# Performance work log

Hardware: AMD Instinct MI355X
Metric: run time of the kernel (lower is better)

## Reference

```python
import jax, jax.numpy as jnp
import numpy as np

D = 1024
H = 16
DH = D // H
F = 4096
B, S = 4, 2048
EPS = 1e-5


def _ln(x, g, b):
    m = jnp.mean(x, axis=-1, keepdims=True)
    v = jnp.var(x, axis=-1, keepdims=True)
    return (x - m) * jax.lax.rsqrt(v + EPS) * g + b


def setup_inputs() -> dict:
    key = jax.random.key(0)
    ks = jax.random.split(key, 16)
    s = 0.02
    return {
        "x": jax.random.normal(ks[0], (B, S, D), jnp.float32),
        "key_padding_mask": jnp.zeros((B, S), jnp.bool_),
        "Wq": jax.random.normal(ks[1], (D, D), jnp.float32) * s,
        "bq": jnp.zeros((D,), jnp.float32),
        "Wk": jax.random.normal(ks[2], (D, D), jnp.float32) * s,
        "bk": jnp.zeros((D,), jnp.float32),
        "Wv": jax.random.normal(ks[3], (D, D), jnp.float32) * s,
        "bv": jnp.zeros((D,), jnp.float32),
        "Wo": jax.random.normal(ks[4], (D, D), jnp.float32) * s,
        "bo": jnp.zeros((D,), jnp.float32),
        "W1": jax.random.normal(ks[5], (F, D), jnp.float32) * s,
        "b1": jnp.zeros((F,), jnp.float32),
        "W2": jax.random.normal(ks[6], (D, F), jnp.float32) * s,
        "b2": jnp.zeros((D,), jnp.float32),
        "ln1_g": jnp.ones((D,), jnp.float32),
        "ln1_b": jnp.zeros((D,), jnp.float32),
        "ln2_g": jnp.ones((D,), jnp.float32),
        "ln2_b": jnp.zeros((D,), jnp.float32),
    }


def _attn(x, kpm, Wq, bq, Wk, bk, Wv, bv, Wo, bo):
    b, s, d = x.shape
    scaling = DH ** (-0.5)
    q = (x @ Wq.T + bq) * scaling
    k = x @ Wk.T + bk
    v = x @ Wv.T + bv
    q = q.reshape(b, s, H, DH)
    k = k.reshape(b, s, H, DH)
    v = v.reshape(b, s, H, DH)
    # [b,h,q,k]
    scores = jnp.einsum("bqhd,bkhd->bhqk", q, k)
    scores = jnp.where(kpm[:, None, None, :], -jnp.inf, scores)
    p = jax.nn.softmax(scores.astype(jnp.float32), axis=-1).astype(q.dtype)
    out = jnp.einsum("bhqk,bkhd->bqhd", p, v).reshape(b, s, d)
    return out @ Wo.T + bo


def reference(x, key_padding_mask, Wq, bq, Wk, bk, Wv, bv, Wo, bo,
              W1, b1, W2, b2, ln1_g, ln1_b, ln2_g, ln2_b):
    # post-LN (normalize_before=False), dropout in eval mode (identity)
    x = _ln(x + _attn(x, key_padding_mask, Wq, bq, Wk, bk, Wv, bv, Wo, bo), ln1_g, ln1_b)
    h = jax.nn.gelu(x @ W1.T + b1, approximate=False)
    x = _ln(x + (h @ W2.T + b2), ln2_g, ln2_b)
    return x
```

## Files before the change

kernel.cpp:

```cpp
#include <hip/hip_runtime.h>
#include <hip/hip_bf16.h>
#include <math.h>

typedef short bf16x8 __attribute__((ext_vector_type(8)));
typedef float f32x4 __attribute__((ext_vector_type(4)));

__device__ __forceinline__ unsigned short f2bfu(float f) {
    __hip_bfloat16 h = __float2bfloat16(f);
    return __builtin_bit_cast(unsigned short, h);
}

__device__ __forceinline__ float fexp2(float x) {
    float r;
    asm("v_exp_f32 %0, %1" : "=v"(r) : "v"(x));
    return r;
}

__device__ __forceinline__ unsigned cvtpk_bf16(float lo, float hi) {
    unsigned r;
    asm("v_cvt_pk_bf16_f32 %0, %1, %2" : "=v"(r) : "v"(lo), "v"(hi));
    return r;
}

__device__ __forceinline__ float gelu_fast(float x) {
    const float x2 = x * x;
    const float z = x * (0.7978845608f + 0.0356774081f * x2);
    const float e = fexp2(z * 2.88539008f);
    const float r = __builtin_amdgcn_rcpf(e + 1.0f);
    return x * (1.0f - r);
}

__device__ __forceinline__ void gload_lds16(const void* gsrc, void* ldst) {
    __builtin_amdgcn_global_load_lds((const __attribute__((address_space(1))) void*)gsrc,
                                     (__attribute__((address_space(3))) void*)ldst,
                                     16, 0, 0);
}

#define MFMA __builtin_amdgcn_mfma_f32_16x16x32_bf16

__global__ __launch_bounds__(256)
void cvt_bf16_kernel(const float4* __restrict__ in, ushort4* __restrict__ out, int n4) {
    int i = blockIdx.x * 256 + threadIdx.x;
    if (i >= n4) return;
    float4 v = in[i];
    ushort4 o;
    o.x = f2bfu(v.x); o.y = f2bfu(v.y); o.z = f2bfu(v.z); o.w = f2bfu(v.w);
    out[i] = o;
}

enum { EPI_QKV = 0, EPI_RESF32 = 2, EPI_GELU = 3, EPI_RESBF16 = 5 };

template<int EPI>
__global__ __launch_bounds__(256, 2)
void gemm_w(const __hip_bfloat16* __restrict__ A,
            const __hip_bfloat16* __restrict__ W,
            const float* __restrict__ bias,
            const void* __restrict__ resv,
            float scale,
            void* __restrict__ outp, void* __restrict__ outp2, void* __restrict__ outp3,
            int M, int N, int K)
{
    __shared__ __hip_bfloat16 As[3][128 * 32];
    __shared__ __hip_bfloat16 Ws[3][256 * 32];
    const int tid = threadIdx.x;
    const int lane = tid & 63;
    const int w = tid >> 6;
    const int g = lane >> 4, lr = lane & 15;
    const int row0 = blockIdx.x * 128;
    const int col0 = blockIdx.y * 256;

    f32x4 acc[8][4];
    const f32x4 zero = {0.f, 0.f, 0.f, 0.f};
#pragma unroll
    for (int m = 0; m < 8; ++m)
#pragma unroll
        for (int n = 0; n < 4; ++n) acc[m][n] = zero;

    const int ra0 = tid >> 2;
    const int ra1 = (tid + 256) >> 2;
    const int ka0 = (((tid) & 3) ^ ((ra0 >> 1) & 3)) * 8;
    const int ka1 = (((tid) & 3) ^ ((ra1 >> 1) & 3)) * 8;
    const int rw0 = ra0, rw1 = ra1;
    const int rw2 = (tid + 512) >> 2;
    const int rw3 = (tid + 768) >> 2;
    const int kw2 = (((tid) & 3) ^ ((rw2 >> 1) & 3)) * 8;
    const int kw3 = (((tid) & 3) ^ ((rw3 >> 1) & 3)) * 8;

    const __hip_bfloat16* Aa0 = A + (size_t)(row0 + ra0) * K + ka0;
    const __hip_bfloat16* Aa1 = A + (size_t)(row0 + ra1) * K + ka1;
    const __hip_bfloat16* Ww0 = W + (size_t)(col0 + rw0) * K + ka0;
    const __hip_bfloat16* Ww1 = W + (size_t)(col0 + rw1) * K + ka1;
    const __hip_bfloat16* Ww2 = W + (size_t)(col0 + rw2) * K + kw2;
    const __hip_bfloat16* Ww3 = W + (size_t)(col0 + rw3) * K + kw3;

    auto stage = [&](int bi, int k0) {
        gload_lds16(Aa0 + k0, (char*)As[bi] + tid * 16);
        gload_lds16(Aa1 + k0, (char*)As[bi] + (tid + 256) * 16);
        gload_lds16(Ww0 + k0, (char*)Ws[bi] + tid * 16);
        gload_lds16(Ww1 + k0, (char*)Ws[bi] + (tid + 256) * 16);
        gload_lds16(Ww2 + k0, (char*)Ws[bi] + (tid + 512) * 16);
        gload_lds16(Ww3 + k0, (char*)Ws[bi] + (tid + 768) * 16);
    };

    const int NT = K >> 5;
    stage(0, 0);
    stage(1, 32);
    asm volatile("s_waitcnt vmcnt(6)" ::: "memory");
    __builtin_amdgcn_s_barrier();
    __builtin_amdgcn_sched_barrier(0);

    const int swl = (lr >> 1) & 3;
    int cur = 0, stg = 2, kpre = 64;

    for (int t = 0; t < NT; ++t) {
        if (t + 2 < NT) stage(stg, kpre);

        bf16x8 af[8], wf[4];
#pragma unroll
        for (int m = 0; m < 8; ++m)
            af[m] = *(const bf16x8*)(As[cur] + (m * 16 + lr) * 32 + (g ^ swl) * 8);
#pragma unroll
        for (int n = 0; n < 4; ++n)
            wf[n] = *(const bf16x8*)(Ws[cur] + (w * 64 + n * 16 + lr) * 32 + (g ^ swl) * 8);
#pragma unroll
        for (int m = 0; m < 8; ++m)
#pragma unroll
            for (int n = 0; n < 4; ++n)
                acc[m][n] = MFMA(af[m], wf[n], acc[m][n], 0, 0, 0);

        if (t + 1 < NT) {
            if (t + 2 < NT) asm volatile("s_waitcnt vmcnt(6)" ::: "memory");
            else            asm volatile("s_waitcnt vmcnt(0)" ::: "memory");
            __builtin_amdgcn_s_barrier();
            __builtin_amdgcn_sched_barrier(0);
        }
        cur = (cur == 2) ? 0 : cur + 1;
        stg = (stg == 2) ? 0 : stg + 1;
        kpre += 32;
    }

#pragma unroll
    for (int n = 0; n < 4; ++n) {
        const int cc = col0 + w * 64 + n * 16 + lr;
        const float bv = bias[cc];
#pragma unroll
        for (int m = 0; m < 8; ++m) {
            const int rbase = row0 + m * 16 + g * 4;
            if (EPI == EPI_QKV) {
                const int seg = col0 >> 10;
                if (seg == 2) {
                    ushort4 u;
                    u.x = f2bfu(acc[m][n][0] + bv);
                    u.y = f2bfu(acc[m][n][1] + bv);
                    u.z = f2bfu(acc[m][n][2] + bv);
                    u.w = f2bfu(acc[m][n][3] + bv);
                    const int cc2 = cc - 2048;
                    const int h_ = cc2 >> 6, dh = cc2 & 63;
                    const int bb = rbase >> 11;
                    const int s = rbase & 2047;
                    *(ushort4*)((__hip_bfloat16*)outp3 +
                                (((size_t)bb * 16 + h_) * 64 + dh) * 2048 + s) = u;
                } else {
                    const float sc = (seg == 0) ? scale : 1.0f;
                    __hip_bfloat16* dst = (seg == 0) ? (__hip_bfloat16*)outp
                                                     : (__hip_bfloat16*)outp2;
                    const int ccl = cc & 1023;
#pragma unroll
                    for (int r = 0; r < 4; ++r)
                        dst[(size_t)(rbase + r) * 1024 + ccl] =
                            __float2bfloat16((acc[m][n][r] + bv) * sc);
                }
            } else {
#pragma unroll
                for (int r = 0; r < 4; ++r) {
                    const size_t idx = (size_t)(rbase + r) * N + cc;
                    float v = acc[m][n][r] + bv;
                    if (EPI == EPI_RESF32) {
                        ((float*)outp)[idx] = v + ((const float*)resv)[idx];
                    } else if (EPI == EPI_RESBF16) {
                        ((float*)outp)[idx] = v +
                            __bfloat162float(((const __hip_bfloat16*)resv)[idx]);
                    } else if (EPI == EPI_GELU) {
                        ((__hip_bfloat16*)outp)[idx] = __float2bfloat16(gelu_fast(v));
                    }
                }
            }
        }
    }
}

template<int EPI>
__global__ __launch_bounds__(256, 3)
void gemm_bt(const __hip_bfloat16* __restrict__ A,
             const __hip_bfloat16* __restrict__ W,
             const float* __restrict__ bias,
             const void* __restrict__ resv,
             float scale,
             void* __restrict__ outp, void* __restrict__ outp2, void* __restrict__ outp3,
             int M, int N, int K)
{
    __shared__ __hip_bfloat16 As[3][128 * 32];
    __shared__ __hip_bfloat16 Ws[3][128 * 32];
    const int tid = threadIdx.x;
    const int lane = tid & 63;
    const int wid = tid >> 6;
    const int wr = wid >> 1, wc = wid & 1;
    const int g = lane >> 4, lr = lane & 15;
    const int row0 = blockIdx.x * 128;
    const int col0 = blockIdx.y * 128;

    f32x4 acc[4][4];
    const f32x4 zero = {0.f, 0.f, 0.f, 0.f};
#pragma unroll
    for (int m = 0; m < 4; ++m)
#pragma unroll
        for (int n = 0; n < 4; ++n) acc[m][n] = zero;

    const int c0 = tid, c1 = tid + 256;
    const int ar0 = c0 >> 2, ac0 = (c0 & 3) * 8;
    const int ar1 = c1 >> 2, ac1 = (c1 & 3) * 8;
    const __hip_bfloat16* Arow0 = A + (size_t)(row0 + ar0) * K + ac0;
    const __hip_bfloat16* Arow1 = A + (size_t)(row0 + ar1) * K + ac1;
    const __hip_bfloat16* Wrow0 = W + (size_t)(col0 + ar0) * K + ac0;
    const __hip_bfloat16* Wrow1 = W + (size_t)(col0 + ar1) * K + ac1;

    auto stage = [&](int bi, int k0) {
        gload_lds16(Arow0 + k0, (char*)As[bi] + c0 * 16);
        gload_lds16(Arow1 + k0, (char*)As[bi] + c1 * 16);
        gload_lds16(Wrow0 + k0, (char*)Ws[bi] + c0 * 16);
        gload_lds16(Wrow1 + k0, (char*)Ws[bi] + c1 * 16);
    };

    const int NT = K >> 5;
    stage(0, 0);
    stage(1, 32);
    asm volatile("s_waitcnt vmcnt(4)" ::: "memory");
    __builtin_amdgcn_s_barrier();
    __builtin_amdgcn_sched_barrier(0);

    int cur = 0, stg = 2;
    int kpre = 64;
    for (int t = 0; t < NT; ++t) {
        if (t + 2 < NT) stage(stg, kpre);

        bf16x8 af[4], wf[4];
#pragma unroll
        for (int m = 0; m < 4; ++m)
            af[m] = *(const bf16x8*)(As[cur] + (wr * 64 + m * 16 + lr) * 32 + g * 8);
#pragma unroll
        for (int n = 0; n < 4; ++n)
            wf[n] = *(const bf16x8*)(Ws[cur] + (wc * 64 + n * 16 + lr) * 32 + g * 8);
#pragma unroll
        for (int m = 0; m < 4; ++m)
#pragma unroll
            for (int n = 0; n < 4; ++n)
                acc[m][n] = MFMA(af[m], wf[n], acc[m][n], 0, 0, 0);

        if (t + 1 < NT) {
            if (t + 2 < NT) asm volatile("s_waitcnt vmcnt(4)" ::: "memory");
            else            asm volatile("s_waitcnt vmcnt(0)" ::: "memory");
            __builtin_amdgcn_s_barrier();
            __builtin_amdgcn_sched_barrier(0);
        }
        cur = (cur == 2) ? 0 : cur + 1;
        stg = (stg == 2) ? 0 : stg + 1;
        kpre += 32;
    }

#pragma unroll
    for (int n = 0; n < 4; ++n) {
        const int cc = col0 + wc * 64 + n * 16 + lr;
        const float bv = bias[cc];
#pragma unroll
        for (int m = 0; m < 4; ++m) {
            const int rbase = row0 + wr * 64 + m * 16 + g * 4;
#pragma unroll
            for (int r = 0; r < 4; ++r) {
                const size_t idx = (size_t)(rbase + r) * N + cc;
                float v = acc[m][n][r] + bv;
                if (EPI == EPI_RESF32) {
                    ((float*)outp)[idx] = v + ((const float*)resv)[idx];
                } else if (EPI == EPI_RESBF16) {
                    ((float*)outp)[idx] = v +
                        __bfloat162float(((const __hip_bfloat16*)resv)[idx]);
                } else if (EPI == EPI_GELU) {
                    ((__hip_bfloat16*)outp)[idx] = __float2bfloat16(gelu_fast(v));
                }
            }
        }
    }
}

__global__ __launch_bounds__(256, 2)
void attn_flash2(const __hip_bfloat16* __restrict__ Q,
                 const __hip_bfloat16* __restrict__ K,
                 const __hip_bfloat16* __restrict__ VT,
                 const unsigned char* __restrict__ kpm,
                 __hip_bfloat16* __restrict__ O)
{
    __shared__ __hip_bfloat16 Ks[2][64 * 64];
    __shared__ __hip_bfloat16 VTs[2][64 * 64];
    __shared__ __hip_bfloat16 Plds[4][64 * 64];

    const int tid = threadIdx.x;
    const int lane = tid & 63;
    const int w = tid >> 6;
    const int g = lane >> 4, lr = lane & 15;

    const int orig = blockIdx.y * 8 + blockIdx.x;
    const int nl = (orig & 7) * 64 + (orig >> 3);
    const int qb = nl & 7;
    const int bh = nl >> 3;

    const int b = bh >> 4, h = bh & 15;
    const int q0 = qb * 256 + w * 64;
    const size_t tokbase = (size_t)b * 2048;
    const __hip_bfloat16* VTbh = VT + (size_t)bh * 64 * 2048;

    unsigned tmask = 0;
#pragma unroll
    for (int i = 0; i < 8; ++i) {
        const unsigned mv = *(const unsigned*)(kpm + tokbase + i * 256 + lane * 4);
        const unsigned long long bal = __ballot((int)(mv != 0u));
#pragma unroll
        for (int j = 0; j < 4; ++j)
            if ((bal >> (16 * j)) & 0xFFFFull) tmask |= (1u << (i * 4 + j));
    }

    bf16x8 qf[4][2];
#pragma unroll
    for (int qn = 0; qn < 4; ++qn)
#pragma unroll
        for (int f = 0; f < 2; ++f)
            qf[qn][f] = *(const bf16x8*)(Q + (tokbase + q0 + qn * 16 + lr) * 1024 +
                                         h * 64 + f * 32 + g * 8);

    f32x4 o[4][4];
    const f32x4 zero = {0.f, 0.f, 0.f, 0.f};
#pragma unroll
    for (int qa = 0; qa < 4; ++qa)
#pragma unroll
        for (int nd = 0; nd < 4; ++nd) o[qa][nd] = zero;
    float m_run[4], l_part[4];
#pragma unroll
    for (int qn = 0; qn < 4; ++qn) { m_run[qn] = -1e30f; l_part[qn] = 0.f; }

    __hip_bfloat16* Pw = Plds[w];
    const int rowl = lane >> 3;
    const int blkp = lane & 7;

    auto stage = [&](int bufi, int kv0) {
#pragma unroll
        for (int iss = 0; iss < 2; ++iss) {
            const int row = w * 16 + iss * 8 + rowl;
            const int sblk = blkp ^ (row & 7);
            gload_lds16(K + (tokbase + kv0 + row) * 1024 + h * 64 + sblk * 8,
                        (char*)&Ks[bufi][(w * 16 + iss * 8) * 64] + lane * 16);
            gload_lds16(VTbh + (size_t)row * 2048 + kv0 + sblk * 8,
                        (char*)&VTs[bufi][(w * 16 + iss * 8) * 64] + lane * 16);
        }
    };

    stage(0, 0);
    __syncthreads();
    int buf = 0;

    for (int t = 0; t < 32; ++t) {
        const int kv0 = t * 64;
        if (t < 31) stage(buf ^ 1, kv0 + 64);

        f32x4 st[4][4];
        __builtin_amdgcn_s_setprio(1);
#pragma unroll
        for (int km = 0; km < 4; ++km) {
            bf16x8 kf[2];
#pragma unroll
            for (int f = 0; f < 2; ++f)
                kf[f] = *(const bf16x8*)(&Ks[buf][(km * 16 + lr) * 64 +
                                                  (((f * 4 + g) ^ (lr & 7)) * 8)]);
#pragma unroll
            for (int qn = 0; qn < 4; ++qn) {
                st[km][qn] = MFMA(kf[0], qf[qn][0], zero, 0, 0, 0);
                st[km][qn] = MFMA(kf[1], qf[qn][1], st[km][qn], 0, 0, 0);
            }
        }
        __builtin_amdgcn_s_setprio(0);

        if (tmask & (1u << t)) {
            const float NEG = -1e30f;
#pragma unroll
            for (int km = 0; km < 4; ++km) {
                const unsigned mu = *(const unsigned*)(kpm + tokbase + kv0 + km * 16 + g * 4);
#pragma unroll
                for (int r = 0; r < 4; ++r) {
                    if ((mu >> (8 * r)) & 0xFFu) {
#pragma unroll
                        for (int qn = 0; qn < 4; ++qn) st[km][qn][r] = NEG;
                    }
                }
            }
        }

        float pm[4];
#pragma unroll
        for (int qn = 0; qn < 4; ++qn) {
            float a0 = fmaxf(fmaxf(st[0][qn][0], st[0][qn][1]), fmaxf(st[0][qn][2], st[0][qn][3]));
            float a1 = fmaxf(fmaxf(st[1][qn][0], st[1][qn][1]), fmaxf(st[1][qn][2], st[1][qn][3]));
            float a2 = fmaxf(fmaxf(st[2][qn][0], st[2][qn][1]), fmaxf(st[2][qn][2], st[2][qn][3]));
            float a3 = fmaxf(fmaxf(st[3][qn][0], st[3][qn][1]), fmaxf(st[3][qn][2], st[3][qn][3]));
            pm[qn] = fmaxf(fmaxf(a0, a1), fmaxf(a2, a3));
        }
        const int trig = (pm[0] > m_run[0] + 8.f) | (pm[1] > m_run[1] + 8.f) |
                         (pm[2] > m_run[2] + 8.f) | (pm[3] > m_run[3] + 8.f);
        if (__any(trig)) {
            float alpha_q[4];
#pragma unroll
            for (int qn = 0; qn < 4; ++qn) {
                float rm = pm[qn];
                rm = fmaxf(rm, __shfl_xor(rm, 16));
                rm = fmaxf(rm, __shfl_xor(rm, 32));
                const float mnew = fmaxf(m_run[qn], rm);
                const float al = fexp2(m_run[qn] - mnew);
                l_part[qn] *= al;
                m_run[qn] = mnew;
                alpha_q[qn] = al;
            }
#pragma unroll
            for (int qa = 0; qa < 4; ++qa)
#pragma unroll
                for (int r = 0; r < 4; ++r) {
                    const float av = __shfl(alpha_q[qa], g * 4 + r, 16);
#pragma unroll
                    for (int nd = 0; nd < 4; ++nd) o[qa][nd][r] *= av;
                }
        }

#pragma unroll
        for (int qn = 0; qn < 4; ++qn) {
            const float mm = m_run[qn];
#pragma unroll
            for (int km = 0; km < 4; ++km) {
                const float p0 = fexp2(st[km][qn][0] - mm);
                const float p1 = fexp2(st[km][qn][1] - mm);
                const float p2 = fexp2(st[km][qn][2] - mm);
                const float p3 = fexp2(st[km][qn][3] - mm);
                l_part[qn] += (p0 + p1) + (p2 + p3);
                uint2 pk;
                pk.x = cvtpk_bf16(p0, p1);
                pk.y = cvtpk_bf16(p2, p3);
                const int cs = (km * 2 + (g >> 1)) ^ (lr & 7);
                *(uint2*)(Pw + (qn * 16 + lr) * 64 + cs * 8 + (g & 1) * 4) = pk;
            }
        }

        __builtin_amdgcn_s_setprio(1);
#pragma unroll
        for (int f = 0; f < 2; ++f) {
            bf16x8 pa[4];
#pragma unroll
            for (int qa = 0; qa < 4; ++qa)
                pa[qa] = *(const bf16x8*)(Pw + (qa * 16 + lr) * 64 +
                                          (((f * 4 + g) ^ (lr & 7)) * 8));
#pragma unroll
            for (int nd = 0; nd < 4; ++nd) {
                bf16x8 vb = *(const bf16x8*)(&VTs[buf][(nd * 16 + lr) * 64 +
                                                       (((f * 4 + g) ^ (lr & 7)) * 8)]);
#pragma unroll
                for (int qa = 0; qa < 4; ++qa)
                    o[qa][nd] = MFMA(pa[qa], vb, o[qa][nd], 0, 0, 0);
            }
        }
        __builtin_amdgcn_s_setprio(0);

        __syncthreads();
        buf ^= 1;
    }

    float linv[4];
#pragma unroll
    for (int qn = 0; qn < 4; ++qn) {
        float lt = l_part[qn];
        lt += __shfl_xor(lt, 16);
        lt += __shfl_xor(lt, 32);
        linv[qn] = 1.0f / lt;
    }
#pragma unroll
    for (int qa = 0; qa < 4; ++qa)
#pragma unroll
        for (int r = 0; r < 4; ++r) {
            const float lv = __shfl(linv[qa], g * 4 + r, 16);
            const size_t row = tokbase + q0 + qa * 16 + g * 4 + r;
#pragma unroll
            for (int nd = 0; nd < 4; ++nd)
                O[row * 1024 + h * 64 + nd * 16 + lr] = __float2bfloat16(o[qa][nd][r] * lv);
        }
}

__global__ __launch_bounds__(256)
void ln_kernel(const float* __restrict__ in, const float* __restrict__ gamma,
               const float* __restrict__ beta, float* __restrict__ outf,
               __hip_bfloat16* __restrict__ outb)
{
    const int row = blockIdx.x;
    const int tid = threadIdx.x;
    float4 v = ((const float4*)(in + (size_t)row * 1024))[tid];
    float s = v.x + v.y + v.z + v.w;
    float s2 = v.x * v.x + v.y * v.y + v.z * v.z + v.w * v.w;
#pragma unroll
    for (int off = 1; off < 64; off <<= 1) {
        s += __shfl_xor(s, off);
        s2 += __shfl_xor(s2, off);
    }
    __shared__ float red[8];
    const int wv = tid >> 6;
    if ((tid & 63) == 0) { red[wv] = s; red[4 + wv] = s2; }
    __syncthreads();
    s = red[0] + red[1] + red[2] + red[3];
    s2 = red[4] + red[5] + red[6] + red[7];
    const float mean = s * (1.f / 1024.f);
    const float var = s2 * (1.f / 1024.f) - mean * mean;
    const float rstd = rsqrtf(var + 1e-5f);
    float4 gm = ((const float4*)gamma)[tid];
    float4 bt = ((const float4*)beta)[tid];
    float4 y;
    y.x = (v.x - mean) * rstd * gm.x + bt.x;
    y.y = (v.y - mean) * rstd * gm.y + bt.y;
    y.z = (v.z - mean) * rstd * gm.z + bt.z;
    y.w = (v.w - mean) * rstd * gm.w + bt.w;
    if (outf) ((float4*)(outf + (size_t)row * 1024))[tid] = y;
    if (outb) {
        ushort4 ub;
        ub.x = f2bfu(y.x); ub.y = f2bfu(y.y); ub.z = f2bfu(y.z); ub.w = f2bfu(y.w);
        ((ushort4*)outb)[row * 256 + tid] = ub;
    }
}

extern "C" void kernel_launch(void* const* d_in, const int* in_sizes, int n_in,
                              void* d_out, int out_size, void* d_ws, size_t ws_size,
                              hipStream_t stream)
{
    const float* x    = (const float*)d_in[0];
    const unsigned char* kpm = (const unsigned char*)d_in[1];
    const float* Wq = (const float*)d_in[2];
    const float* bq = (const float*)d_in[3];
    const float* Wk = (const float*)d_in[4];
    const float* bk = (const float*)d_in[5];
    const float* Wv = (const float*)d_in[6];
    const float* bv = (const float*)d_in[7];
    const float* Wo = (const float*)d_in[8];
    const float* bo = (const float*)d_in[9];
    const float* W1 = (const float*)d_in[10];
    const float* b1 = (const float*)d_in[11];
    const float* W2 = (const float*)d_in[12];
    const float* b2 = (const float*)d_in[13];
    const float* ln1g = (const float*)d_in[14];
    const float* ln1b = (const float*)d_in[15];
    const float* ln2g = (const float*)d_in[16];
    const float* ln2b = (const float*)d_in[17];
    float* out = (float*)d_out;

    char* ws = (char*)d_ws;
    const size_t SZ_ND2 = (size_t)8192 * 1024 * 2;
    size_t off = 0;
    __hip_bfloat16* xb  = (__hip_bfloat16*)(ws + off); off += SZ_ND2;
    __hip_bfloat16* wqb = (__hip_bfloat16*)(ws + off); off += (size_t)1024 * 1024 * 2;
    __hip_bfloat16* wkb = (__hip_bfloat16*)(ws + off); off += (size_t)1024 * 1024 * 2;
    __hip_bfloat16* wvb = (__hip_bfloat16*)(ws + off); off += (size_t)1024 * 1024 * 2;
    __hip_bfloat16* wob = (__hip_bfloat16*)(ws + off); off += (size_t)1024 * 1024 * 2;
    __hip_bfloat16* w1b = (__hip_bfloat16*)(ws + off); off += (size_t)4096 * 1024 * 2;
    __hip_bfloat16* w2b = (__hip_bfloat16*)(ws + off); off += (size_t)4096 * 1024 * 2;
    const size_t qkv0 = off;
    __hip_bfloat16* qbp = (__hip_bfloat16*)(ws + off); off += SZ_ND2;
    __hip_bfloat16* kbp = (__hip_bfloat16*)(ws + off); off += SZ_ND2;
    __hip_bfloat16* vtg = (__hip_bfloat16*)(ws + off); off += SZ_ND2;
    __hip_bfloat16* abp = (__hip_bfloat16*)(ws + off); off += SZ_ND2;
    __hip_bfloat16* hbp = (__hip_bfloat16*)(ws + qkv0);
    float* y1 = (float*)(ws + off); off += (size_t)8192 * 1024 * 4;
    __hip_bfloat16* x1b = (__hip_bfloat16*)(ws + off); off += SZ_ND2;
    float* y2 = y1;
    float* bqkv = (float*)(ws + off); off += 3072 * 4;

    auto cvt = [&](const float* src, void* dst, int n) {
        cvt_bf16_kernel<<<n / 1024, 256, 0, stream>>>((const float4*)src, (ushort4*)dst, n / 4);
    };
    cvt(x,  xb,  8192 * 1024);
    cvt(Wq, wqb, 1024 * 1024);
    cvt(Wk, wkb, 1024 * 1024);
    cvt(Wv, wvb, 1024 * 1024);
    cvt(Wo, wob, 1024 * 1024);
    cvt(W1, w1b, 4096 * 1024);
    cvt(W2, w2b, 4096 * 1024);
    hipMemcpyAsync(bqkv,        bq, 4096, hipMemcpyDeviceToDevice, stream);
    hipMemcpyAsync(bqkv + 1024, bk, 4096, hipMemcpyDeviceToDevice, stream);
    hipMemcpyAsync(bqkv + 2048, bv, 4096, hipMemcpyDeviceToDevice, stream);

    dim3 blk(256);
    const float qscale = 0.125f * 1.44269504088896f;

    gemm_w<EPI_QKV><<<dim3(64, 12), blk, 0, stream>>>(
        xb, wqb, bqkv, nullptr, qscale, qbp, kbp, vtg, 8192, 3072, 1024);

    attn_flash2<<<dim3(8, 64), blk, 0, stream>>>(qbp, kbp, vtg, kpm, abp);

    gemm_bt<EPI_RESF32><<<dim3(64, 8), blk, 0, stream>>>(
        abp, wob, bo, x, 1.0f, y1, nullptr, nullptr, 8192, 1024, 1024);
    ln_kernel<<<8192, 256, 0, stream>>>(y1, ln1g, ln1b, nullptr, x1b);

    gemm_w<EPI_GELU><<<dim3(64, 16), blk, 0, stream>>>(
        x1b, w1b, b1, nullptr, 1.0f, hbp, nullptr, nullptr, 8192, 4096, 1024);
    gemm_bt<EPI_RESBF16><<<dim3(64, 8), blk, 0, stream>>>(
        hbp, w2b, b2, x1b, 1.0f, y2, nullptr, nullptr, 8192, 1024, 4096);
    ln_kernel<<<8192, 256, 0, stream>>>(y2, ln2g, ln2b, out, nullptr);
}
```

Measured before the change: 449.1 us.

## Add 256x256 eight-wave GEMM for FFN1 and route QKV through 128x128 kernel

```diff
diff --git a/kernel.cpp b/kernel.cpp
--- a/kernel.cpp
+++ b/kernel.cpp
@@ -51,85 +51,192 @@
 enum { EPI_QKV = 0, EPI_RESF32 = 2, EPI_GELU = 3, EPI_RESBF16 = 5 };
 
 template<int EPI>
-__global__ __launch_bounds__(256, 2)
-void gemm_w(const __hip_bfloat16* __restrict__ A,
-            const __hip_bfloat16* __restrict__ W,
-            const float* __restrict__ bias,
-            const void* __restrict__ resv,
-            float scale,
-            void* __restrict__ outp, void* __restrict__ outp2, void* __restrict__ outp3,
-            int M, int N, int K)
+__global__ __launch_bounds__(512, 4)
+void gemm2(const __hip_bfloat16* __restrict__ A,
+           const __hip_bfloat16* __restrict__ W,
+           const float* __restrict__ bias,
+           const void* __restrict__ resv,
+           float scale,
+           void* __restrict__ outp,
+           int M, int N, int K)
+{
+    __shared__ __hip_bfloat16 As[2][256 * 32];
+    __shared__ __hip_bfloat16 Bs[2][256 * 32];
+    const int tid = threadIdx.x;
+    const int lane = tid & 63;
+    const int wid = tid >> 6;
+    const int wr = wid >> 2;
+    const int wc = wid & 3;
+    const int g = lane >> 4, lr = lane & 15;
+    const int row0 = blockIdx.x * 256;
+    const int col0 = blockIdx.y * 256;
+
+    const int r0 = tid >> 2;
+    const int r1 = r0 + 128;
+    const int c0s = tid & 3;
+    const int ca0 = (c0s ^ ((r0 >> 1) & 3)) * 8;
+    const int ca1 = (c0s ^ ((r1 >> 1) & 3)) * 8;
+    const __hip_bfloat16* Aa0 = A + (size_t)(row0 + r0) * K + ca0;
+    const __hip_bfloat16* Aa1 = A + (size_t)(row0 + r1) * K + ca1;
+    const __hip_bfloat16* Wb0 = W + (size_t)(col0 + r0) * K + ca0;
+    const __hip_bfloat16* Wb1 = W + (size_t)(col0 + r1) * K + ca1;
+
+    auto stageA = [&](int bi, int k0) {
+        gload_lds16(Aa0 + k0, (char*)As[bi] + tid * 16);
+        gload_lds16(Aa1 + k0, (char*)As[bi] + tid * 16 + 8192);
+    };
+    auto stageB = [&](int bi, int k0) {
+        gload_lds16(Wb0 + k0, (char*)Bs[bi] + tid * 16);
+        gload_lds16(Wb1 + k0, (char*)Bs[bi] + tid * 16 + 8192);
+    };
+
+    f32x4 acc[8][4];
+    const f32x4 zero = {0.f, 0.f, 0.f, 0.f};
+#pragma unroll
+    for (int m = 0; m < 8; ++m)
+#pragma unroll
+        for (int n = 0; n < 4; ++n) acc[m][n] = zero;
+
+    const int NT = K >> 5;
+    stageA(0, 0);
+    stageB(0, 0);
+    asm volatile("s_waitcnt vmcnt(0)" ::: "memory");
+    __builtin_amdgcn_s_barrier();
+    __builtin_amdgcn_sched_barrier(0);
+
+    const int swl = (lr >> 1) & 3;
+
+    for (int t = 0; t < NT; ++t) {
+        const int buf = t & 1;
+        const int kn = (t + 1) * 32;
+        bf16x8 a[4], b[4];
+
+#pragma unroll
+        for (int m = 0; m < 4; ++m)
+            a[m] = *(const bf16x8*)(As[buf] + (wr * 128 + m * 16 + lr) * 32 + (g ^ swl) * 8);
+#pragma unroll
+        for (int n = 0; n < 4; ++n)
+            b[n] = *(const bf16x8*)(Bs[buf] + (wc * 64 + n * 16 + lr) * 32 + (g ^ swl) * 8);
+        if (t + 1 < NT) { stageA(buf ^ 1, kn); stageB(buf ^ 1, kn); }
+        __builtin_amdgcn_s_barrier();
+        __builtin_amdgcn_s_setprio(1);
+#pragma unroll
+        for (int m = 0; m < 4; ++m)
+#pragma unroll
+            for (int n = 0; n < 4; ++n)
+                acc[m][n] = MFMA(a[m], b[n], acc[m][n], 0, 0, 0);
+        __builtin_amdgcn_s_setprio(0);
+        __builtin_amdgcn_s_barrier();
+
+#pragma unroll
+        for (int m = 0; m < 4; ++m)
+            a[m] = *(const bf16x8*)(As[buf] + (wr * 128 + (m + 4) * 16 + lr) * 32 + (g ^ swl) * 8);
+        __builtin_amdgcn_s_barrier();
+        __builtin_amdgcn_s_setprio(1);
+#pragma unroll
+        for (int m = 0; m < 4; ++m)
+#pragma unroll
+            for (int n = 0; n < 4; ++n)
+                acc[m + 4][n] = MFMA(a[m], b[n], acc[m + 4][n], 0, 0, 0);
+        __builtin_amdgcn_s_setprio(0);
+        asm volatile("s_waitcnt vmcnt(0)" ::: "memory");
+        __builtin_amdgcn_s_barrier();
+        __builtin_amdgcn_sched_barrier(0);
+    }
+
+#pragma unroll
+    for (int n = 0; n < 4; ++n) {
+        const int cc = col0 + wc * 64 + n * 16 + lr;
+        const float bv = bias[cc];
+#pragma unroll
+        for (int m = 0; m < 8; ++m) {
+            const int rbase = row0 + wr * 128 + m * 16 + g * 4;
+#pragma unroll
+            for (int r = 0; r < 4; ++r) {
+                const size_t idx = (size_t)(rbase + r) * N + cc;
+                float v = acc[m][n][r] + bv;
+                if (EPI == EPI_RESF32) {
+                    ((float*)outp)[idx] = v + ((const float*)resv)[idx];
+                } else if (EPI == EPI_RESBF16) {
+                    ((float*)outp)[idx] = v +
+                        __bfloat162float(((const __hip_bfloat16*)resv)[idx]);
+                } else if (EPI == EPI_GELU) {
+                    ((__hip_bfloat16*)outp)[idx] = __float2bfloat16(gelu_fast(v));
+                }
+            }
+        }
+    }
+}
+
+template<int EPI>
+__global__ __launch_bounds__(256, 3)
+void gemm_bt(const __hip_bfloat16* __restrict__ A,
+             const __hip_bfloat16* __restrict__ W,
+             const float* __restrict__ bias,
+             const void* __restrict__ resv,
+             float scale,
+             void* __restrict__ outp, void* __restrict__ outp2, void* __restrict__ outp3,
+             int M, int N, int K)
 {
     __shared__ __hip_bfloat16 As[3][128 * 32];
-    __shared__ __hip_bfloat16 Ws[3][256 * 32];
+    __shared__ __hip_bfloat16 Ws[3][128 * 32];
     const int tid = threadIdx.x;
     const int lane = tid & 63;
-    const int w = tid >> 6;
+    const int wid = tid >> 6;
+    const int wr = wid >> 1, wc = wid & 1;
     const int g = lane >> 4, lr = lane & 15;
     const int row0 = blockIdx.x * 128;
-    const int col0 = blockIdx.y * 256;
-
-    f32x4 acc[8][4];
+    const int col0 = blockIdx.y * 128;
+
+    f32x4 acc[4][4];
     const f32x4 zero = {0.f, 0.f, 0.f, 0.f};
 #pragma unroll
-    for (int m = 0; m < 8; ++m)
+    for (int m = 0; m < 4; ++m)
 #pragma unroll
         for (int n = 0; n < 4; ++n) acc[m][n] = zero;
 
-    const int ra0 = tid >> 2;
-    const int ra1 = (tid + 256) >> 2;
-    const int ka0 = (((tid) & 3) ^ ((ra0 >> 1) & 3)) * 8;
-    const int ka1 = (((tid) & 3) ^ ((ra1 >> 1) & 3)) * 8;
-    const int rw0 = ra0, rw1 = ra1;
-    const int rw2 = (tid + 512) >> 2;
-    const int rw3 = (tid + 768) >> 2;
-    const int kw2 = (((tid) & 3) ^ ((rw2 >> 1) & 3)) * 8;
-    const int kw3 = (((tid) & 3) ^ ((rw3 >> 1) & 3)) * 8;
-
-    const __hip_bfloat16* Aa0 = A + (size_t)(row0 + ra0) * K + ka0;
-    const __hip_bfloat16* Aa1 = A + (size_t)(row0 + ra1) * K + ka1;
-    const __hip_bfloat16* Ww0 = W + (size_t)(col0 + rw0) * K + ka0;
-    const __hip_bfloat16* Ww1 = W + (size_t)(col0 + rw1) * K + ka1;
-    const __hip_bfloat16* Ww2 = W + (size_t)(col0 + rw2) * K + kw2;
-    const __hip_bfloat16* Ww3 = W + (size_t)(col0 + rw3) * K + kw3;
+    const int c0 = tid, c1 = tid + 256;
+    const int ar0 = c0 >> 2, ac0 = (c0 & 3) * 8;
+    const int ar1 = c1 >> 2, ac1 = (c1 & 3) * 8;
+    const __hip_bfloat16* Arow0 = A + (size_t)(row0 + ar0) * K + ac0;
+    const __hip_bfloat16* Arow1 = A + (size_t)(row0 + ar1) * K + ac1;
+    const __hip_bfloat16* Wrow0 = W + (size_t)(col0 + ar0) * K + ac0;
+    const __hip_bfloat16* Wrow1 = W + (size_t)(col0 + ar1) * K + ac1;
 
     auto stage = [&](int bi, int k0) {
-        gload_lds16(Aa0 + k0, (char*)As[bi] + tid * 16);
-        gload_lds16(Aa1 + k0, (char*)As[bi] + (tid + 256) * 16);
-        gload_lds16(Ww0 + k0, (char*)Ws[bi] + tid * 16);
-        gload_lds16(Ww1 + k0, (char*)Ws[bi] + (tid + 256) * 16);
-        gload_lds16(Ww2 + k0, (char*)Ws[bi] + (tid + 512) * 16);
-        gload_lds16(Ww3 + k0, (char*)Ws[bi] + (tid + 768) * 16);
+        gload_lds16(Arow0 + k0, (char*)As[bi] + c0 * 16);
+        gload_lds16(Arow1 + k0, (char*)As[bi] + c1 * 16);
+        gload_lds16(Wrow0 + k0, (char*)Ws[bi] + c0 * 16);
+        gload_lds16(Wrow1 + k0, (char*)Ws[bi] + c1 * 16);
     };
 
     const int NT = K >> 5;
     stage(0, 0);
     stage(1, 32);
-    asm volatile("s_waitcnt vmcnt(6)" ::: "memory");
+    asm volatile("s_waitcnt vmcnt(4)" ::: "memory");
     __builtin_amdgcn_s_barrier();
     __builtin_amdgcn_sched_barrier(0);
 
-    const int swl = (lr >> 1) & 3;
-    int cur = 0, stg = 2, kpre = 64;
-
+    int cur = 0, stg = 2;
+    int kpre = 64;
     for (int t = 0; t < NT; ++t) {
         if (t + 2 < NT) stage(stg, kpre);
 
-        bf16x8 af[8], wf[4];
-#pragma unroll
-        for (int m = 0; m < 8; ++m)
-            af[m] = *(const bf16x8*)(As[cur] + (m * 16 + lr) * 32 + (g ^ swl) * 8);
+        bf16x8 af[4], wf[4];
+#pragma unroll
+        for (int m = 0; m < 4; ++m)
+            af[m] = *(const bf16x8*)(As[cur] + (wr * 64 + m * 16 + lr) * 32 + g * 8);
 #pragma unroll
         for (int n = 0; n < 4; ++n)
-            wf[n] = *(const bf16x8*)(Ws[cur] + (w * 64 + n * 16 + lr) * 32 + (g ^ swl) * 8);
-#pragma unroll
-        for (int m = 0; m < 8; ++m)
+            wf[n] = *(const bf16x8*)(Ws[cur] + (wc * 64 + n * 16 + lr) * 32 + g * 8);
+#pragma unroll
+        for (int m = 0; m < 4; ++m)
 #pragma unroll
             for (int n = 0; n < 4; ++n)
                 acc[m][n] = MFMA(af[m], wf[n], acc[m][n], 0, 0, 0);
 
         if (t + 1 < NT) {
-            if (t + 2 < NT) asm volatile("s_waitcnt vmcnt(6)" ::: "memory");
+            if (t + 2 < NT) asm volatile("s_waitcnt vmcnt(4)" ::: "memory");
             else            asm volatile("s_waitcnt vmcnt(0)" ::: "memory");
             __builtin_amdgcn_s_barrier();
             __builtin_amdgcn_sched_barrier(0);
@@ -141,11 +248,11 @@
 
 #pragma unroll
     for (int n = 0; n < 4; ++n) {
-        const int cc = col0 + w * 64 + n * 16 + lr;
+        const int cc = col0 + wc * 64 + n * 16 + lr;
         const float bv = bias[cc];
 #pragma unroll
-        for (int m = 0; m < 8; ++m) {
-            const int rbase = row0 + m * 16 + g * 4;
+        for (int m = 0; m < 4; ++m) {
+            const int rbase = row0 + wr * 64 + m * 16 + g * 4;
             if (EPI == EPI_QKV) {
                 const int seg = col0 >> 10;
                 if (seg == 2) {
@@ -183,108 +290,6 @@
                     } else if (EPI == EPI_GELU) {
                         ((__hip_bfloat16*)outp)[idx] = __float2bfloat16(gelu_fast(v));
                     }
-                }
-            }
-        }
-    }
-}
-
-template<int EPI>
-__global__ __launch_bounds__(256, 3)
-void gemm_bt(const __hip_bfloat16* __restrict__ A,
-             const __hip_bfloat16* __restrict__ W,
-             const float* __restrict__ bias,
-             const void* __restrict__ resv,
-             float scale,
-             void* __restrict__ outp, void* __restrict__ outp2, void* __restrict__ outp3,
-             int M, int N, int K)
-{
-    __shared__ __hip_bfloat16 As[3][128 * 32];
-    __shared__ __hip_bfloat16 Ws[3][128 * 32];
-    const int tid = threadIdx.x;
-    const int lane = tid & 63;
-    const int wid = tid >> 6;
-    const int wr = wid >> 1, wc = wid & 1;
-    const int g = lane >> 4, lr = lane & 15;
-    const int row0 = blockIdx.x * 128;
-    const int col0 = blockIdx.y * 128;
-
-    f32x4 acc[4][4];
-    const f32x4 zero = {0.f, 0.f, 0.f, 0.f};
-#pragma unroll
-    for (int m = 0; m < 4; ++m)
-#pragma unroll
-        for (int n = 0; n < 4; ++n) acc[m][n] = zero;
-
-    const int c0 = tid, c1 = tid + 256;
-    const int ar0 = c0 >> 2, ac0 = (c0 & 3) * 8;
-    const int ar1 = c1 >> 2, ac1 = (c1 & 3) * 8;
-    const __hip_bfloat16* Arow0 = A + (size_t)(row0 + ar0) * K + ac0;
-    const __hip_bfloat16* Arow1 = A + (size_t)(row0 + ar1) * K + ac1;
-    const __hip_bfloat16* Wrow0 = W + (size_t)(col0 + ar0) * K + ac0;
-    const __hip_bfloat16* Wrow1 = W + (size_t)(col0 + ar1) * K + ac1;
-
-    auto stage = [&](int bi, int k0) {
-        gload_lds16(Arow0 + k0, (char*)As[bi] + c0 * 16);
-        gload_lds16(Arow1 + k0, (char*)As[bi] + c1 * 16);
-        gload_lds16(Wrow0 + k0, (char*)Ws[bi] + c0 * 16);
-        gload_lds16(Wrow1 + k0, (char*)Ws[bi] + c1 * 16);
-    };
-
-    const int NT = K >> 5;
-    stage(0, 0);
-    stage(1, 32);
-    asm volatile("s_waitcnt vmcnt(4)" ::: "memory");
-    __builtin_amdgcn_s_barrier();
-    __builtin_amdgcn_sched_barrier(0);
-
-    int cur = 0, stg = 2;
-    int kpre = 64;
-    for (int t = 0; t < NT; ++t) {
-        if (t + 2 < NT) stage(stg, kpre);
-
-        bf16x8 af[4], wf[4];
-#pragma unroll
-        for (int m = 0; m < 4; ++m)
-            af[m] = *(const bf16x8*)(As[cur] + (wr * 64 + m * 16 + lr) * 32 + g * 8);
-#pragma unroll
-        for (int n = 0; n < 4; ++n)
-            wf[n] = *(const bf16x8*)(Ws[cur] + (wc * 64 + n * 16 + lr) * 32 + g * 8);
-#pragma unroll
-        for (int m = 0; m < 4; ++m)
-#pragma unroll
-            for (int n = 0; n < 4; ++n)
-                acc[m][n] = MFMA(af[m], wf[n], acc[m][n], 0, 0, 0);
-
-        if (t + 1 < NT) {
-            if (t + 2 < NT) asm volatile("s_waitcnt vmcnt(4)" ::: "memory");
-            else            asm volatile("s_waitcnt vmcnt(0)" ::: "memory");
-            __builtin_amdgcn_s_barrier();
-            __builtin_amdgcn_sched_barrier(0);
-        }
-        cur = (cur == 2) ? 0 : cur + 1;
-        stg = (stg == 2) ? 0 : stg + 1;
-        kpre += 32;
-    }
-
-#pragma unroll
-    for (int n = 0; n < 4; ++n) {
-        const int cc = col0 + wc * 64 + n * 16 + lr;
-        const float bv = bias[cc];
-#pragma unroll
-        for (int m = 0; m < 4; ++m) {
-            const int rbase = row0 + wr * 64 + m * 16 + g * 4;
-#pragma unroll
-            for (int r = 0; r < 4; ++r) {
-                const size_t idx = (size_t)(rbase + r) * N + cc;
-                float v = acc[m][n][r] + bv;
-                if (EPI == EPI_RESF32) {
-                    ((float*)outp)[idx] = v + ((const float*)resv)[idx];
-                } else if (EPI == EPI_RESBF16) {
-                    ((float*)outp)[idx] = v +
-                        __bfloat162float(((const __hip_bfloat16*)resv)[idx]);
-                } else if (EPI == EPI_GELU) {
-                    ((__hip_bfloat16*)outp)[idx] = __float2bfloat16(gelu_fast(v));
                 }
             }
         }
@@ -597,7 +602,7 @@
     dim3 blk(256);
     const float qscale = 0.125f * 1.44269504088896f;
 
-    gemm_w<EPI_QKV><<<dim3(64, 12), blk, 0, stream>>>(
+    gemm_bt<EPI_QKV><<<dim3(64, 24), blk, 0, stream>>>(
         xb, wqb, bqkv, nullptr, qscale, qbp, kbp, vtg, 8192, 3072, 1024);
 
     attn_flash2<<<dim3(8, 64), blk, 0, stream>>>(qbp, kbp, vtg, kpm, abp);
@@ -606,8 +611,8 @@
         abp, wob, bo, x, 1.0f, y1, nullptr, nullptr, 8192, 1024, 1024);
     ln_kernel<<<8192, 256, 0, stream>>>(y1, ln1g, ln1b, nullptr, x1b);
 
-    gemm_w<EPI_GELU><<<dim3(64, 16), blk, 0, stream>>>(
-        x1b, w1b, b1, nullptr, 1.0f, hbp, nullptr, nullptr, 8192, 4096, 1024);
+    gemm2<EPI_GELU><<<dim3(32, 16), 512, 0, stream>>>(
+        x1b, w1b, b1, nullptr, 1.0f, hbp, 8192, 4096, 1024);
     gemm_bt<EPI_RESBF16><<<dim3(64, 8), blk, 0, stream>>>(
         hbp, w2b, b2, x1b, 1.0f, y2, nullptr, nullptr, 8192, 1024, 4096);
     ln_kernel<<<8192, 256, 0, stream>>>(y2, ln2g, ln2b, out, nullptr);
```

Measured after the change: 949.9 us. 2.11x slower.
